# Optimization experiments

Hardware: AMD Instinct MI355X
Metric: run time of the kernel (lower is better)

The kernel has to match this reference:

```python
import jax, jax.numpy as jnp
import numpy as np

N_NODES = 100000
N_EDGES = 3200000
N_FEAT = 128
HIDDEN = 16
N_CLASSES = 10
N_GRAPHS = 64


def gcn_conv(x, W, b, src, dst, num_nodes):
    # PyG GCNConv: h = x W; add self-loops; norm = deg^{-1/2}[src]*deg^{-1/2}[dst]
    h = x @ W  # [N, out]
    deg = jax.ops.segment_sum(jnp.ones(src.shape[0], h.dtype), dst,
                              num_segments=num_nodes) + 1.0  # self-loop
    dinv = jax.lax.rsqrt(deg)
    coef = dinv[src] * dinv[dst]  # [E]
    agg = jax.ops.segment_sum(h[src] * coef[:, None], dst,
                              num_segments=num_nodes)
    # self-loop contribution: norm = dinv[i]^2
    agg = agg + h * (dinv * dinv)[:, None]
    return agg + b


def setup_inputs() -> dict:
    key = jax.random.key(0)
    k1, k2, k3, k4, k5, k6, k7 = jax.random.split(key, 7)
    x = jax.random.normal(k1, (N_NODES, N_FEAT), dtype=jnp.float32)
    edge_index = jax.random.randint(k2, (2, N_EDGES), 0, N_NODES, dtype=jnp.int64)
    batch = jnp.sort(jax.random.randint(k3, (N_NODES,), 0, N_GRAPHS, dtype=jnp.int64))
    W1 = jax.random.normal(k4, (N_FEAT, HIDDEN), dtype=jnp.float32) / np.sqrt(N_FEAT)
    b1 = jnp.zeros((HIDDEN,), jnp.float32)
    W2 = jax.random.normal(k5, (HIDDEN, N_CLASSES), dtype=jnp.float32) / np.sqrt(HIDDEN)
    b2 = jnp.zeros((N_CLASSES,), jnp.float32)
    return {"x": x, "edge_index": edge_index, "batch": batch,
            "W1": W1, "b1": b1, "W2": W2, "b2": b2}


def reference(x, edge_index, batch, W1, b1, W2, b2):
    src, dst = edge_index[0], edge_index[1]
    h = gcn_conv(x, W1, b1, src, dst, N_NODES)
    h = jax.nn.relu(h)
    h = gcn_conv(h, W2, b2, src, dst, N_NODES)  # [N, C]
    # global mean pool per graph
    sums = jax.ops.segment_sum(h, batch, num_segments=N_GRAPHS)
    cnts = jax.ops.segment_sum(jnp.ones(N_NODES, h.dtype), batch,
                               num_segments=N_GRAPHS)
    pooled = sums / jnp.maximum(cnts, 1.0)[:, None]  # [G, C]
    return jax.nn.log_softmax(pooled, axis=1)
```

## Files before the change

kernel.cpp:

```cpp
#include <hip/hip_runtime.h>
#include <hip/hip_fp16.h>

#define N_NODES   100000
#define N_EDGES   3200000
#define N_FEAT    128
#define HIDDEN    16
#define N_CLASSES 10
#define N_GRAPHS  64

#define NBUCK     391
#define CAP       9216
#define SLOT      64
#define ROWCAP    88
#define BINA_EPB  8192
#define BINA_BLOCKS ((N_EDGES + BINA_EPB - 1) / BINA_EPB)


__global__ __launch_bounds__(1024) void k_binA(const int* __restrict__ src,
                                               const int* __restrict__ dst,
                                               int* __restrict__ gcnt,
                                               int* __restrict__ stage,
                                               float* __restrict__ pooled) {
    __shared__ int curb[NBUCK];
    int tid = threadIdx.x;
    int cellbase = blockIdx.x * NBUCK;
    for (int t = tid; t < NBUCK; t += 1024) curb[t] = (cellbase + t) * SLOT;
    if (blockIdx.x == 0) pooled[tid] = 0.f;
    __syncthreads();
    long long base = (long long)blockIdx.x * BINA_EPB;
#pragma unroll
    for (int p = 0; p < 2; ++p) {
        long long e0 = base + p * 4096 + tid * 4;
        if (e0 < N_EDGES) {
            int4 s4 = *(const int4*)&src[e0];
            int4 d4 = *(const int4*)&dst[e0];
            int p0 = atomicAdd(&curb[d4.x >> 8], 1);
            int p1 = atomicAdd(&curb[d4.y >> 8], 1);
            int p2 = atomicAdd(&curb[d4.z >> 8], 1);
            int p3 = atomicAdd(&curb[d4.w >> 8], 1);
            stage[p0] = (s4.x << 8) | (d4.x & 255);
            stage[p1] = (s4.y << 8) | (d4.y & 255);
            stage[p2] = (s4.z << 8) | (d4.z & 255);
            stage[p3] = (s4.w << 8) | (d4.w & 255);
        }
    }
    __syncthreads();
    for (int t = tid; t < NBUCK; t += 1024)
        gcnt[cellbase + t] = curb[t] - (cellbase + t) * SLOT;
}

__global__ __launch_bounds__(1024) void k_binB(const int* __restrict__ gcnt,
                                               const int* __restrict__ stage,
                                               int2* __restrict__ be,
                                               float* __restrict__ dinv,
                                               int* __restrict__ srcs) {
    __shared__ int rows[256][ROWCAP];
    __shared__ int cur[256];
    __shared__ int excl[256];
    __shared__ int scnt[BINA_BLOCKS];
    int b = blockIdx.x, tid = threadIdx.x;
    if (tid < 256) cur[tid] = 0;
    for (int s = tid; s < BINA_BLOCKS; s += 1024) scnt[s] = gcnt[s * NBUCK + b];
    __syncthreads();
    int stream = tid >> 5, ln = tid & 31;
    for (int s = stream; s < BINA_BLOCKS; s += 32) {
        int c  = scnt[s];
        int sb = (s * NBUCK + b) * SLOT;
        for (int i = ln; i < c; i += 32) {
            int v = stage[sb + i];
            int nloc = v & 255;
            int p = atomicAdd(&cur[nloc], 1);
            rows[nloc][p] = v >> 8;
        }
    }
    __syncthreads();
    int c = 0;
    if (tid < 256) { c = cur[tid]; excl[tid] = c; }
    __syncthreads();
    for (int o = 1; o < 256; o <<= 1) {
        int a = 0;
        if (tid < 256 && tid >= o) a = excl[tid - o];
        __syncthreads();
        if (tid < 256) excl[tid] += a;
        __syncthreads();
    }
    int sbase = b * CAP;
    if (tid < 256) {
        int ex = excl[tid] - c;
        int node = b * 256 + tid;
        if (node < N_NODES) {
            be[node]   = make_int2(sbase + ex, sbase + ex + c);
            dinv[node] = rsqrtf((float)c + 1.0f);
        }
    }
    __syncthreads();
    int g = tid >> 2, j = tid & 3;
    int cg = cur[g];
    int ob = sbase + excl[g] - cg;
    for (int i = j; i < cg; i += 4) srcs[ob + i] = rows[g][i];
}

__global__ __launch_bounds__(256) void k_gemm1(const float* __restrict__ x,
                                               const float* __restrict__ W1,
                                               const float* __restrict__ dinv,
                                               __half* __restrict__ h1h) {
    __shared__ float wT[16][132];
    __shared__ float xs[16 * N_FEAT];
    __shared__ float ds[16];
    int tid  = threadIdx.x;
    int base = blockIdx.x * 16;
    if (tid < 16) ds[tid] = dinv[base + tid];
    const float4* w4 = (const float4*)W1;
    float4 wa = w4[tid], wb = w4[256 + tid];
    {
        int r = tid >> 2, cb = (tid & 3) * 4;
        wT[cb + 0][r] = wa.x; wT[cb + 1][r] = wa.y;
        wT[cb + 2][r] = wa.z; wT[cb + 3][r] = wa.w;
        int r2 = r + 64;
        wT[cb + 0][r2] = wb.x; wT[cb + 1][r2] = wb.y;
        wT[cb + 2][r2] = wb.z; wT[cb + 3][r2] = wb.w;
    }
    const float4* x4 = (const float4*)(x + (long long)base * N_FEAT);
    float4*       xd = (float4*)xs;
    xd[tid]       = x4[tid];
    xd[256 + tid] = x4[256 + tid];
    __syncthreads();
    int n = tid >> 4, c = tid & 15;
    const float4* xv = (const float4*)&xs[n * N_FEAT];
    const float4* wv = (const float4*)&wT[c][0];
    float acc = 0.f;
#pragma unroll
    for (int k4 = 0; k4 < 32; ++k4) {
        float4 a = xv[k4], w = wv[k4];
        acc += a.x * w.x + a.y * w.y + a.z * w.z + a.w * w.w;
    }
    h1h[(base + n) * HIDDEN + c] = __float2half(acc * ds[n]);
}

#define NT(p) __builtin_nontemporal_load(p)

#define GATHER_DEF(TBL)                                                       \
    float acc[8];                                                             \
    _Pragma("unroll") for (int q = 0; q < 8; ++q) acc[q] = 0.f;               \
    {                                                                         \
        int ne = end - beg;                                                   \
        int nr = ne >> 3;                                                     \
        int j  = beg + k;                                                     \
        int npair = nr >> 1;                                                  \
        if (npair > 0) {                                                      \
            int sA = NT(&srcs[j]), sB = NT(&srcs[j + 8]);                     \
            for (int p = 1; p < npair; ++p) {                                 \
                int sC = NT(&srcs[j + 16]), sD = NT(&srcs[j + 24]);           \
                GACC(TBL, sA); GACC(TBL, sB);                                 \
                sA = sC; sB = sD; j += 16;                                    \
            }                                                                 \
            GACC(TBL, sA); GACC(TBL, sB); j += 16;                            \
        }                                                                     \
        if (nr & 1) { int sA = NT(&srcs[j]); GACC(TBL, sA); j += 8; }         \
        if (k < (ne & 7)) { int sA = NT(&srcs[j]); GACC(TBL, sA); }           \
    }                                                                         \
    _Pragma("unroll") for (int m = 2; m <= 8; m <<= 1) {                      \
        _Pragma("unroll") for (int q = 0; q < 8; ++q)                         \
            acc[q] += __shfl_xor(acc[q], m, 64);                              \
    }

#define GACC(TBL, S) {                                                        \
    float4 g_ = *(const float4*)(&TBL[(S) * 16 + h * 8]);                     \
    const __half2* hp_ = (const __half2*)&g_;                                 \
    float2 v0_ = __half22float2(hp_[0]);                                      \
    float2 v1_ = __half22float2(hp_[1]);                                      \
    float2 v2_ = __half22float2(hp_[2]);                                      \
    float2 v3_ = __half22float2(hp_[3]);                                      \
    acc[0] += v0_.x; acc[1] += v0_.y; acc[2] += v1_.x; acc[3] += v1_.y;       \
    acc[4] += v2_.x; acc[5] += v2_.y; acc[6] += v3_.x; acc[7] += v3_.y; }

__global__ __launch_bounds__(256) void k_agg1(const int2* __restrict__ be,
                                              const int* __restrict__ srcs,
                                              const float* __restrict__ dinv,
                                              const __half* __restrict__ h1h,
                                              const float* __restrict__ b1,
                                              const float* __restrict__ W2,
                                              __half* __restrict__ h2h) {
    __shared__ float r_s[16][17];
    __shared__ float w2s[HIDDEN * N_CLASSES];
    int tid = threadIdx.x;
    if (tid < HIDDEN * N_CLASSES) w2s[tid] = W2[tid];
    int nl = tid >> 4, l = tid & 15, k = l >> 1, h = l & 1;
    int n  = blockIdx.x * 16 + nl;
    int2 bn = be[n];
    int beg = bn.x, end = bn.y;
    GATHER_DEF(h1h)
    if (l < 2) {
#pragma unroll
        for (int q = 0; q < 8; ++q) r_s[nl][h * 8 + q] = acc[q];
    }
    __syncthreads();
    float dn   = dinv[n];
    float self = __half2float(h1h[n * 16 + l]);
    float val  = fmaxf(dn * (r_s[nl][l] + self) + b1[l], 0.f);
    __syncthreads();
    r_s[nl][l] = val;
    __syncthreads();
    float o = 0.f;
    if (l < N_CLASSES) {
#pragma unroll
        for (int q = 0; q < HIDDEN; ++q) o += r_s[nl][q] * w2s[q * N_CLASSES + l];
        o *= dn;
    }
    h2h[n * 16 + l] = __float2half(o);
}

__global__ __launch_bounds__(256) void k_agg2p(const int2* __restrict__ be,
                                               const int* __restrict__ srcs,
                                               const float* __restrict__ dinv,
                                               const __half* __restrict__ h2h,
                                               const int* __restrict__ batch,
                                               float* __restrict__ pooled) {
    __shared__ float red[16][17];
    int tid = threadIdx.x;
    int nl = tid >> 4, l = tid & 15, k = l >> 1, h = l & 1;
    int nbase = blockIdx.x * 16;
    int n  = nbase + nl;
    int2 bn = be[n];
    int beg = bn.x, end = bn.y;
    GATHER_DEF(h2h)
    if (l < 2) {
#pragma unroll
        for (int q = 0; q < 8; ++q) red[nl][h * 8 + q] = acc[q];
    }
    __syncthreads();
    float self = __half2float(h2h[n * 16 + l]);
    float o = dinv[n] * (red[nl][l] + self);
    __syncthreads();

    int g0  = batch[nbase];
    int g15 = batch[nbase + 15];
    if (g0 == g15) {
        red[nl][l] = o;
        __syncthreads();
#pragma unroll
        for (int s = 8; s > 0; s >>= 1) {
            if (nl < s) red[nl][l] += red[nl + s][l];
            __syncthreads();
        }
        if (tid < N_CLASSES) atomicAdd(&pooled[g0 * 16 + tid], red[0][tid]);
    } else {
        if (l < N_CLASSES) atomicAdd(&pooled[batch[n] * 16 + l], o);
    }
}

__global__ __launch_bounds__(64) void k_final(const float* __restrict__ pooled,
                                              const float* __restrict__ b2,
                                              const int* __restrict__ batch,
                                              float* __restrict__ out) {
    int g = threadIdx.x;
    if (g >= N_GRAPHS) return;
    int lo = 0, hi = N_NODES;
    while (lo < hi) { int m = (lo + hi) >> 1; if (batch[m] < g) lo = m + 1; else hi = m; }
    int start = lo;
    lo = 0; hi = N_NODES;
    while (lo < hi) { int m = (lo + hi) >> 1; if (batch[m] < g + 1) lo = m + 1; else hi = m; }
    int cnt = lo - start;

    float v[N_CLASSES];
    if (cnt > 0) {
        float inv = 1.f / (float)cnt;
#pragma unroll
        for (int j = 0; j < N_CLASSES; ++j) v[j] = pooled[g * 16 + j] * inv + b2[j];
    } else {
#pragma unroll
        for (int j = 0; j < N_CLASSES; ++j) v[j] = 0.f;
    }
    float m = v[0];
#pragma unroll
    for (int j = 1; j < N_CLASSES; ++j) m = fmaxf(m, v[j]);
    float l = 0.f;
#pragma unroll
    for (int j = 0; j < N_CLASSES; ++j) l += expf(v[j] - m);
    l = logf(l);
#pragma unroll
    for (int j = 0; j < N_CLASSES; ++j) out[g * N_CLASSES + j] = v[j] - m - l;
}

extern "C" void kernel_launch(void* const* d_in, const int* in_sizes, int n_in,
                              void* d_out, int out_size, void* d_ws, size_t ws_size,
                              hipStream_t stream) {
    const float* x     = (const float*)d_in[0];
    const int*   edge  = (const int*)d_in[1];
    const int*   batch = (const int*)d_in[2];
    const float* W1    = (const float*)d_in[3];
    const float* b1    = (const float*)d_in[4];
    const float* W2    = (const float*)d_in[5];
    const float* b2    = (const float*)d_in[6];
    float* out = (float*)d_out;
    float* ws  = (float*)d_ws;

    float*  pooled = ws;
    float*  dinv   = ws + 1024;
    int2*   be     = (int2*)(ws + 101024);
    int*    gcnt   = (int*)(ws + 301024);
    int*    srcs   = (int*)(ws + 454912);
    int*    stage  = (int*)(ws + 4058368);
    __half* h1h    = (__half*)(ws + 4058368);
    __half* h2h    = (__half*)(ws + 4858368);

    const int* srcp = edge;
    const int* dstp = edge + N_EDGES;

    k_binA<<<BINA_BLOCKS, 1024, 0, stream>>>(srcp, dstp, gcnt, stage, pooled);
    k_binB<<<NBUCK, 1024, 0, stream>>>(gcnt, stage, be, dinv, srcs);
    k_gemm1<<<N_NODES / 16, 256, 0, stream>>>(x, W1, dinv, h1h);
    k_agg1<<<N_NODES / 16, 256, 0, stream>>>(be, srcs, dinv, h1h, b1, W2, h2h);
    k_agg2p<<<N_NODES / 16, 256, 0, stream>>>(be, srcs, dinv, h2h, batch, pooled);
    k_final<<<1, 64, 0, stream>>>(pooled, b2, batch, out);
}
```

Before: 227.6 us.

## Fuse final log-softmax into agg2p via last-block and retune edge binning

The separate single-block k_final launch is removed. Its pooling-normalisation and log-softmax now run in the last-finishing k_agg2p block, detected with a global atomic counter and thread fences, and pooled values are read back through atomics. Edge binning is also retuned: half as many edges per k_binA block, a smaller per-cell staging slot, and narrower 16-lane streams in k_binB so more streams walk the doubled number of cells. This saves a kernel launch and changes the parallelism of the binning phase, at the cost of more gcnt cells and a larger staging footprint.

Result: slower. 711.6 us (+212.7%).

```diff
diff --git a/kernel.cpp b/kernel.cpp
--- a/kernel.cpp
+++ b/kernel.cpp
@@ -10,39 +10,40 @@
 
 #define NBUCK     391
 #define CAP       9216
-#define SLOT      64
+#define SLOT      48
 #define ROWCAP    88
-#define BINA_EPB  8192
+#define BINA_EPB  4096
 #define BINA_BLOCKS ((N_EDGES + BINA_EPB - 1) / BINA_EPB)
+#define AGG_BLOCKS (N_NODES / 16)
 
 
 __global__ __launch_bounds__(1024) void k_binA(const int* __restrict__ src,
                                                const int* __restrict__ dst,
                                                int* __restrict__ gcnt,
                                                int* __restrict__ stage,
-                                               float* __restrict__ pooled) {
+                                               float* __restrict__ pooled,
+                                               int* __restrict__ done) {
     __shared__ int curb[NBUCK];
     int tid = threadIdx.x;
     int cellbase = blockIdx.x * NBUCK;
     for (int t = tid; t < NBUCK; t += 1024) curb[t] = (cellbase + t) * SLOT;
-    if (blockIdx.x == 0) pooled[tid] = 0.f;
-    __syncthreads();
-    long long base = (long long)blockIdx.x * BINA_EPB;
-#pragma unroll
-    for (int p = 0; p < 2; ++p) {
-        long long e0 = base + p * 4096 + tid * 4;
-        if (e0 < N_EDGES) {
-            int4 s4 = *(const int4*)&src[e0];
-            int4 d4 = *(const int4*)&dst[e0];
-            int p0 = atomicAdd(&curb[d4.x >> 8], 1);
-            int p1 = atomicAdd(&curb[d4.y >> 8], 1);
-            int p2 = atomicAdd(&curb[d4.z >> 8], 1);
-            int p3 = atomicAdd(&curb[d4.w >> 8], 1);
-            stage[p0] = (s4.x << 8) | (d4.x & 255);
-            stage[p1] = (s4.y << 8) | (d4.y & 255);
-            stage[p2] = (s4.z << 8) | (d4.z & 255);
-            stage[p3] = (s4.w << 8) | (d4.w & 255);
-        }
+    if (blockIdx.x == 0) {
+        pooled[tid] = 0.f;
+        if (tid == 0) *done = 0;
+    }
+    __syncthreads();
+    long long e0 = (long long)blockIdx.x * BINA_EPB + tid * 4;
+    if (e0 < N_EDGES) {
+        int4 s4 = *(const int4*)&src[e0];
+        int4 d4 = *(const int4*)&dst[e0];
+        int p0 = atomicAdd(&curb[d4.x >> 8], 1);
+        int p1 = atomicAdd(&curb[d4.y >> 8], 1);
+        int p2 = atomicAdd(&curb[d4.z >> 8], 1);
+        int p3 = atomicAdd(&curb[d4.w >> 8], 1);
+        stage[p0] = (s4.x << 8) | (d4.x & 255);
+        stage[p1] = (s4.y << 8) | (d4.y & 255);
+        stage[p2] = (s4.z << 8) | (d4.z & 255);
+        stage[p3] = (s4.w << 8) | (d4.w & 255);
     }
     __syncthreads();
     for (int t = tid; t < NBUCK; t += 1024)
@@ -62,11 +63,11 @@
     if (tid < 256) cur[tid] = 0;
     for (int s = tid; s < BINA_BLOCKS; s += 1024) scnt[s] = gcnt[s * NBUCK + b];
     __syncthreads();
-    int stream = tid >> 5, ln = tid & 31;
-    for (int s = stream; s < BINA_BLOCKS; s += 32) {
+    int stream = tid >> 4, ln = tid & 15;
+    for (int s = stream; s < BINA_BLOCKS; s += 64) {
         int c  = scnt[s];
         int sb = (s * NBUCK + b) * SLOT;
-        for (int i = ln; i < c; i += 32) {
+        for (int i = ln; i < c; i += 16) {
             int v = stage[sb + i];
             int nloc = v & 255;
             int p = atomicAdd(&cur[nloc], 1);
@@ -215,8 +216,12 @@
                                                const float* __restrict__ dinv,
                                                const __half* __restrict__ h2h,
                                                const int* __restrict__ batch,
-                                               float* __restrict__ pooled) {
+                                               float* __restrict__ pooled,
+                                               int* __restrict__ done,
+                                               const float* __restrict__ b2,
+                                               float* __restrict__ out) {
     __shared__ float red[16][17];
+    __shared__ int lastFlag;
     int tid = threadIdx.x;
     int nl = tid >> 4, l = tid & 15, k = l >> 1, h = l & 1;
     int nbase = blockIdx.x * 16;
@@ -247,39 +252,41 @@
     } else {
         if (l < N_CLASSES) atomicAdd(&pooled[batch[n] * 16 + l], o);
     }
-}
-
-__global__ __launch_bounds__(64) void k_final(const float* __restrict__ pooled,
-                                              const float* __restrict__ b2,
-                                              const int* __restrict__ batch,
-                                              float* __restrict__ out) {
-    int g = threadIdx.x;
-    if (g >= N_GRAPHS) return;
-    int lo = 0, hi = N_NODES;
-    while (lo < hi) { int m = (lo + hi) >> 1; if (batch[m] < g) lo = m + 1; else hi = m; }
-    int start = lo;
-    lo = 0; hi = N_NODES;
-    while (lo < hi) { int m = (lo + hi) >> 1; if (batch[m] < g + 1) lo = m + 1; else hi = m; }
-    int cnt = lo - start;
-
-    float v[N_CLASSES];
-    if (cnt > 0) {
-        float inv = 1.f / (float)cnt;
-#pragma unroll
-        for (int j = 0; j < N_CLASSES; ++j) v[j] = pooled[g * 16 + j] * inv + b2[j];
-    } else {
-#pragma unroll
-        for (int j = 0; j < N_CLASSES; ++j) v[j] = 0.f;
-    }
-    float m = v[0];
-#pragma unroll
-    for (int j = 1; j < N_CLASSES; ++j) m = fmaxf(m, v[j]);
-    float l = 0.f;
-#pragma unroll
-    for (int j = 0; j < N_CLASSES; ++j) l += expf(v[j] - m);
-    l = logf(l);
-#pragma unroll
-    for (int j = 0; j < N_CLASSES; ++j) out[g * N_CLASSES + j] = v[j] - m - l;
+
+    __threadfence();
+    if (tid == 0) lastFlag = (atomicAdd(done, 1) == AGG_BLOCKS - 1);
+    __syncthreads();
+    if (lastFlag) {
+        __threadfence();
+        int g = tid;
+        if (g < N_GRAPHS) {
+            int lo = 0, hi = N_NODES;
+            while (lo < hi) { int m = (lo + hi) >> 1; if (batch[m] < g) lo = m + 1; else hi = m; }
+            int start = lo;
+            lo = 0; hi = N_NODES;
+            while (lo < hi) { int m = (lo + hi) >> 1; if (batch[m] < g + 1) lo = m + 1; else hi = m; }
+            int cnt = lo - start;
+            float v[N_CLASSES];
+            if (cnt > 0) {
+                float inv = 1.f / (float)cnt;
+#pragma unroll
+                for (int j = 0; j < N_CLASSES; ++j)
+                    v[j] = atomicAdd(&pooled[g * 16 + j], 0.f) * inv + b2[j];
+            } else {
+#pragma unroll
+                for (int j = 0; j < N_CLASSES; ++j) v[j] = 0.f;
+            }
+            float m = v[0];
+#pragma unroll
+            for (int j = 1; j < N_CLASSES; ++j) m = fmaxf(m, v[j]);
+            float lsum = 0.f;
+#pragma unroll
+            for (int j = 0; j < N_CLASSES; ++j) lsum += expf(v[j] - m);
+            lsum = logf(lsum);
+#pragma unroll
+            for (int j = 0; j < N_CLASSES; ++j) out[g * N_CLASSES + j] = v[j] - m - lsum;
+        }
+    }
 }
 
 extern "C" void kernel_launch(void* const* d_in, const int* in_sizes, int n_in,
@@ -296,21 +303,21 @@
     float* ws  = (float*)d_ws;
 
     float*  pooled = ws;
-    float*  dinv   = ws + 1024;
-    int2*   be     = (int2*)(ws + 101024);
-    int*    gcnt   = (int*)(ws + 301024);
-    int*    srcs   = (int*)(ws + 454912);
-    int*    stage  = (int*)(ws + 4058368);
-    __half* h1h    = (__half*)(ws + 4058368);
-    __half* h2h    = (__half*)(ws + 4858368);
+    int*    done   = (int*)(ws + 1024);
+    float*  dinv   = ws + 1056;
+    int2*   be     = (int2*)(ws + 101056);
+    int*    gcnt   = (int*)(ws + 301056);
+    int*    srcs   = (int*)(ws + 606848);
+    int*    stage  = (int*)(ws + 4210304);
+    __half* h1h    = (__half*)(ws + 4210304);
+    __half* h2h    = (__half*)(ws + 5010304);
 
     const int* srcp = edge;
     const int* dstp = edge + N_EDGES;
 
-    k_binA<<<BINA_BLOCKS, 1024, 0, stream>>>(srcp, dstp, gcnt, stage, pooled);
+    k_binA<<<BINA_BLOCKS, 1024, 0, stream>>>(srcp, dstp, gcnt, stage, pooled, done);
     k_binB<<<NBUCK, 1024, 0, stream>>>(gcnt, stage, be, dinv, srcs);
     k_gemm1<<<N_NODES / 16, 256, 0, stream>>>(x, W1, dinv, h1h);
     k_agg1<<<N_NODES / 16, 256, 0, stream>>>(be, srcs, dinv, h1h, b1, W2, h2h);
-    k_agg2p<<<N_NODES / 16, 256, 0, stream>>>(be, srcs, dinv, h2h, batch, pooled);
-    k_final<<<1, 64, 0, stream>>>(pooled, b2, batch, out);
-}
+    k_agg2p<<<AGG_BLOCKS, 256, 0, stream>>>(be, srcs, dinv, h2h, batch, pooled, done, b2, out);
+}
```
